# Kernel optimization log

Hardware: AMD Instinct MI355X
Metric: run time of the kernel (lower is better)

Reference implementation:

```python
import jax, jax.numpy as jnp
import numpy as np
from jax import lax

N, D, K = 8192, 512, 16
EPS = 1e-8


def _safe_sqrt(x):
    # sqrt with a guard so vjp is finite at exact zeros (diagonal of dist matrix)
    return jnp.where(x > 0, jnp.sqrt(jnp.maximum(x, 1e-12)), 0.0)


def _pairwise_dist(a):
    # [n, d] -> [n, n] euclidean distances via Gram trick
    sq = jnp.sum(a * a, axis=-1)
    d2 = sq[:, None] + sq[None, :] - 2.0 * (a @ a.T)
    return _safe_sqrt(d2)


def _curvature_proxy(emb, k):
    n = emb.shape[0]
    dists = _pairwise_dist(emb)  # [n, n]
    neg_d, knn_idx = lax.top_k(-dists, k + 1)  # k+1 smallest
    knn_dists = -neg_d[:, 1:]   # drop self [n, k]
    knn_idx = knn_idx[:, 1:]    # [n, k]
    avg_dist_to_neighbors = knn_dists.mean(axis=1)  # [n]

    nb = emb[knn_idx]  # [n, k, d] gathered neighbor embeddings
    nsq = jnp.sum(nb * nb, axis=-1)  # [n, k]
    gram = jnp.einsum('nkd,nld->nkl', nb, nb)  # [n, k, k]
    inter = _safe_sqrt(nsq[:, :, None] + nsq[:, None, :] - 2.0 * gram)

    mask = jnp.triu(jnp.ones((k, k), dtype=bool), 1)
    n_pairs = k * (k - 1) // 2
    inter_mean = jnp.sum(jnp.where(mask, inter, 0.0), axis=(1, 2)) / n_pairs  # [n]

    curvature = inter_mean / (avg_dist_to_neighbors + EPS)
    return curvature, knn_dists


def setup_inputs() -> dict:
    key = jax.random.key(0)
    k1, k2, k3 = jax.random.split(key, 3)
    embeddings = jax.random.normal(k1, (N, D), dtype=jnp.float32)
    ref_curvature = jax.random.uniform(k2, (N,), dtype=jnp.float32)
    ref_distances = jax.random.uniform(k3, (N, K), dtype=jnp.float32)
    return {"embeddings": embeddings, "ref_curvature": ref_curvature,
            "ref_distances": ref_distances}


def reference(embeddings, ref_curvature, ref_distances):
    curr_curv, curr_dists = _curvature_proxy(embeddings, K)
    curvature_loss = jnp.mean((curr_curv - ref_curvature) ** 2)
    scale_loss = (curr_dists.mean() - ref_distances.mean()) ** 2
    return curvature_loss + 0.1 * scale_loss
```

## Files before the change

### kernel.cpp

```cpp
#include <hip/hip_runtime.h>
#include <cfloat>
#include <cmath>
#include <stdint.h>

#define N 8192
#define D 512
#define K 16
#define RB 64
#define JS 2048
#define NSL (N / JS)
#define JT 128
#define NT (JS / JT)
#define KC 64
#define NCH (D / KC)
#define CAP 32
#define PB 64

typedef __bf16 bf16x8 __attribute__((ext_vector_type(8)));
typedef __bf16 bf16x4 __attribute__((ext_vector_type(4)));
typedef float  f32x16 __attribute__((ext_vector_type(16)));
typedef float  f32x4  __attribute__((ext_vector_type(4)));

__global__ __launch_bounds__(256)
void k_cast_sqnorm(const float* __restrict__ emb, float* __restrict__ sq,
                   __bf16* __restrict__ embh, int* __restrict__ kadjG) {
    int row = blockIdx.x * 4 + (threadIdx.x >> 6);
    int lane = threadIdx.x & 63;
    const float4* e = (const float4*)(emb + (size_t)row * D);
    float s = 0.f;
    #pragma unroll
    for (int c = 0; c < 2; c++) {
        float4 v = e[lane + 64 * c];
        s += v.x * v.x + v.y * v.y + v.z * v.z + v.w * v.w;
        bf16x4 h = { (__bf16)v.x, (__bf16)v.y, (__bf16)v.z, (__bf16)v.w };
        *(bf16x4*)&embh[(size_t)row * D + (size_t)(lane + 64 * c) * 4] = h;
    }
    for (int off = 32; off; off >>= 1) s += __shfl_down(s, off, 64);
    if (lane == 0) sq[row] = s;
    if (lane == 1) kadjG[row] = 0x7f7fffff;
}

__global__ __launch_bounds__(512)
void k_knn(const __bf16* __restrict__ embh, const float* __restrict__ sq,
           float* __restrict__ pd2, int* __restrict__ pidx,
           int* __restrict__ kadjG) {
    __shared__ __align__(16) __bf16 As[2][RB][KC + 8];
    __shared__ __align__(16) __bf16 Bs[2][JT][KC + 8];
    __shared__ float svD[RB][CAP + 1];
    __shared__ int   svI[RB][CAP + 1];
    __shared__ float sqr[RB];
    __shared__ float kadj[RB];
    __shared__ int   scount[RB];
    __shared__ int   again2[2];

    const int t   = threadIdx.x;
    const int rg  = blockIdx.x >> 2;
    const int sl  = blockIdx.x & 3;
    const int ib  = rg * RB;
    const int jsb = sl * JS;
    const int lane = t & 63, quad = lane >> 5, l31 = lane & 31;
    const int w  = t >> 6;
    const int wr = (w & 1) * 32;
    const int wc = (w >> 1) * 32;

    const int mrow = t >> 3, tid8 = t & 7;
    float l0 = FLT_MAX, l1 = FLT_MAX;
    int   i0 = 0, i1 = 0;
    float kmx = FLT_MAX;
    int   nfill = 0;

    if (t < RB) {
        sqr[t] = sq[ib + t];
        kadj[t] = FLT_MAX; scount[t] = 0;
    }
    __syncthreads();

    for (int jt = 0; jt < NT; jt++) {
        const int jb = jsb + jt * JT;
        f32x16 acc = {};

        {
            int row = t >> 3, g = t & 7;
            *(uint4*)&As[0][row][g * 8] = *(const uint4*)&embh[(size_t)(ib + row) * D + g * 8];
            #pragma unroll
            for (int q = 0; q < 2; q++) {
                int s = t + 512 * q;
                int brow = s >> 3, bg = s & 7;
                *(uint4*)&Bs[0][brow][bg * 8] = *(const uint4*)&embh[(size_t)(jb + brow) * D + bg * 8];
            }
        }
        __syncthreads();

        uint4 pfA, pfB[2];
        for (int kc = 0; kc < NCH; kc++) {
            const int cur = kc & 1;
            if (kc + 1 < NCH) {
                int k0 = (kc + 1) * KC;
                {
                    int row = t >> 3, g = t & 7;
                    pfA = *(const uint4*)&embh[(size_t)(ib + row) * D + k0 + g * 8];
                }
                #pragma unroll
                for (int q = 0; q < 2; q++) {
                    int s = t + 512 * q; int brow = s >> 3, bg = s & 7;
                    pfB[q] = *(const uint4*)&embh[(size_t)(jb + brow) * D + k0 + bg * 8];
                }
            }
            #pragma unroll
            for (int kk = 0; kk < KC / 16; kk++) {
                int ko = kk * 16 + quad * 8;
                bf16x8 a0 = *(const bf16x8*)&As[cur][wr + l31][ko];
                bf16x8 b0 = *(const bf16x8*)&Bs[cur][wc + l31][ko];
                acc = __builtin_amdgcn_mfma_f32_32x32x16_bf16(a0, b0, acc, 0, 0, 0);
            }
            if (kc + 1 < NCH) {
                {
                    int row = t >> 3, g = t & 7;
                    *(uint4*)&As[cur ^ 1][row][g * 8] = pfA;
                }
                #pragma unroll
                for (int q = 0; q < 2; q++) {
                    int s = t + 512 * q; int brow = s >> 3, bg = s & 7;
                    *(uint4*)&Bs[cur ^ 1][brow][bg * 8] = pfB[q];
                }
            }
            __syncthreads();
        }

        if (t < RB) {
            float g = __int_as_float(kadjG[ib + t]);
            kadj[t] = fminf(kadj[t], g - sqr[t]);
        }
        if (t == 0) again2[0] = 0;
        __syncthreads();

        float sqc0 = sq[jb + wc + l31];
        uint32_t mask = 0;
        int pass = 0;
        while (true) {
            #pragma unroll
            for (int reg = 0; reg < 16; reg++) {
                if ((mask >> reg) & 1) continue;
                int row_l = wr + ((reg & 3) + ((reg >> 2) << 3) + (quad << 2));
                float t2 = sqc0 - 2.f * acc[reg];
                if (t2 < kadj[row_l]) {
                    int j = jb + wc + l31;
                    if (j != ib + row_l) {
                        int p = atomicAdd(&scount[row_l], 1);
                        if (p < CAP) {
                            svD[row_l][p] = t2 + sqr[row_l];
                            svI[row_l][p] = j;
                            mask |= (1u << reg);
                        }
                    }
                }
            }
            __syncthreads();
            {
                int cnt = scount[mrow];
                if (cnt) {
                    int m = cnt < CAP ? cnt : CAP;
                    for (int p = 0; p < m; p++) {
                        float d2 = svD[mrow][p];
                        if (d2 < kmx) {
                            if (nfill < K) {
                                if ((nfill >> 1) == tid8) {
                                    int jv = svI[mrow][p];
                                    if ((nfill & 1) == 0) { l0 = d2; i0 = jv; }
                                    else                  { l1 = d2; i1 = jv; }
                                }
                                nfill++;
                                if (nfill == K) {
                                    float lm = fmaxf(l0, l1);
                                    #pragma unroll
                                    for (int off = 1; off < 8; off <<= 1)
                                        lm = fmaxf(lm, __shfl_xor(lm, off, 64));
                                    kmx = lm;
                                }
                            } else {
                                float mx = l0; int am = 0;
                                if (l1 > mx) { mx = l1; am = 1; }
                                int gam = (tid8 << 1) | am;
                                #pragma unroll
                                for (int off = 1; off < 8; off <<= 1) {
                                    float omx = __shfl_xor(mx, off, 64);
                                    int   oga = __shfl_xor(gam, off, 64);
                                    if (omx > mx || (omx == mx && oga < gam)) { mx = omx; gam = oga; }
                                }
                                if ((gam >> 1) == tid8) {
                                    int jv = svI[mrow][p];
                                    if ((gam & 1) == 0) { l0 = d2; i0 = jv; }
                                    else                { l1 = d2; i1 = jv; }
                                }
                                float lm = fmaxf(l0, l1);
                                #pragma unroll
                                for (int off = 1; off < 8; off <<= 1)
                                    lm = fmaxf(lm, __shfl_xor(lm, off, 64));
                                kmx = lm;
                            }
                        }
                    }
                    if (tid8 == 0) {
                        kadj[mrow] = fminf(kadj[mrow], kmx - sqr[mrow]);
                        scount[mrow] = 0;
                        if (cnt > CAP) again2[pass & 1] = 1;
                    }
                }
            }
            if (t == 0) again2[(pass + 1) & 1] = 0;
            __syncthreads();
            if (!again2[pass & 1]) break;
            pass++;
        }

        if (tid8 == 0 && kmx < FLT_MAX)
            atomicMin(&kadjG[ib + mrow], __float_as_int(kmx));
    }

    {
        size_t base = (size_t)(ib + mrow) * (NSL * K) + sl * K + tid8 * 2;
        pd2[base + 0] = l0; pd2[base + 1] = l1;
        pidx[base + 0] = i0; pidx[base + 1] = i1;
    }
}

__global__ __launch_bounds__(256)
void k_merge(const float* __restrict__ pd2, const int* __restrict__ pidx,
             int* __restrict__ knn, float* __restrict__ row_sum) {
    int row = blockIdx.x * 256 + threadIdx.x;
    float bd[K]; int bi[K];
    #pragma unroll
    for (int q = 0; q < K; q++) { bd[q] = FLT_MAX; bi[q] = 0; }
    float kmx = FLT_MAX;
    const float* pr = pd2 + (size_t)row * (NSL * K);
    const int*   pi = pidx + (size_t)row * (NSL * K);
    for (int s = 0; s < NSL * K; s++) {
        float d2 = pr[s];
        if (d2 < kmx) {
            int am = 0; float mx = bd[0];
            #pragma unroll
            for (int q = 1; q < K; q++) if (bd[q] > mx) { mx = bd[q]; am = q; }
            bd[am] = d2; bi[am] = pi[s];
            mx = bd[0];
            #pragma unroll
            for (int q = 1; q < K; q++) mx = fmaxf(mx, bd[q]);
            kmx = mx;
        }
    }
    float s = 0.f;
    #pragma unroll
    for (int q = 0; q < K; q++) {
        float d2 = bd[q];
        s += (d2 > 0.f) ? sqrtf(fmaxf(d2, 1e-12f)) : 0.f;
        knn[(size_t)row * K + q] = bi[q];
    }
    row_sum[row] = s;
}

__global__ __launch_bounds__(256)
void k_curv(const __bf16* __restrict__ embh, const int* __restrict__ knn_idx,
            const float* __restrict__ row_sum, const float* __restrict__ ref_curv,
            float* __restrict__ curv_err) {
    __shared__ float diagS[4][16];
    const int t = threadIdx.x;
    const int w = t >> 6, lane = t & 63;
    const int i = blockIdx.x * 4 + w;

    const int nidx = knn_idx[(size_t)i * K + (lane & 15)];
    const __bf16* src = embh + (size_t)nidx * D + (lane >> 4) * 8;

    f32x4 acc = {};
    #pragma unroll
    for (int kc = 0; kc < D / 32; kc++) {
        bf16x8 a = *(const bf16x8*)(src + kc * 32);
        acc = __builtin_amdgcn_mfma_f32_16x16x32_bf16(a, a, acc, 0, 0, 0);
    }

    #pragma unroll
    for (int q = 0; q < 4; q++) {
        int r = (lane >> 4) * 4 + q;
        if (r == (lane & 15)) diagS[w][r] = acc[q];
    }
    __syncthreads();

    float s = 0.f;
    #pragma unroll
    for (int q = 0; q < 4; q++) {
        int r = (lane >> 4) * 4 + q, c = lane & 15;
        if (r != c) {
            float d2 = diagS[w][r] + diagS[w][c] - 2.f * acc[q];
            s += (d2 > 0.f) ? sqrtf(fmaxf(d2, 1e-12f)) : 0.f;
        }
    }
    #pragma unroll
    for (int off = 32; off; off >>= 1) s += __shfl_down(s, off, 64);

    if (lane == 0) {
        float inter_mean = (0.5f * s) / 120.f;
        float avg = row_sum[i] / 16.f;
        float curv = inter_mean / (avg + 1e-8f);
        float diff = curv - ref_curv[i];
        curv_err[i] = diff * diff;
    }
}

__global__ __launch_bounds__(256)
void k_part(const float* __restrict__ curv_err, const float* __restrict__ row_sum,
            const float* __restrict__ ref_dist, float* __restrict__ part) {
    const int b = blockIdx.x, t = threadIdx.x;
    const int gid = b * 256 + t;
    const int stride = PB * 256;
    float s1 = 0.f, s2 = 0.f, s3 = 0.f;
    for (int i = gid; i < N; i += stride) { s1 += curv_err[i]; s2 += row_sum[i]; }
    for (int i = gid; i < N * K; i += stride) s3 += ref_dist[i];
    for (int off = 32; off; off >>= 1) {
        s1 += __shfl_down(s1, off, 64);
        s2 += __shfl_down(s2, off, 64);
        s3 += __shfl_down(s3, off, 64);
    }
    __shared__ float a1[4], a2[4], a3[4];
    int w = t >> 6, lane = t & 63;
    if (lane == 0) { a1[w] = s1; a2[w] = s2; a3[w] = s3; }
    __syncthreads();
    if (t == 0) {
        float t1 = 0.f, t2 = 0.f, t3 = 0.f;
        #pragma unroll
        for (int q = 0; q < 4; q++) { t1 += a1[q]; t2 += a2[q]; t3 += a3[q]; }
        part[b] = t1; part[PB + b] = t2; part[2 * PB + b] = t3;
    }
}

__global__ __launch_bounds__(64)
void k_final2(const float* __restrict__ part, float* __restrict__ out) {
    const int t = threadIdx.x;
    float s1 = part[t], s2 = part[PB + t], s3 = part[2 * PB + t];
    for (int off = 32; off; off >>= 1) {
        s1 += __shfl_down(s1, off, 64);
        s2 += __shfl_down(s2, off, 64);
        s3 += __shfl_down(s3, off, 64);
    }
    if (t == 0) {
        float curv_loss = s1 / (float)N;
        float dm = s2 / (float)(N * K);
        float rm = s3 / (float)(N * K);
        float d = dm - rm;
        out[0] = curv_loss + 0.1f * d * d;
    }
}

extern "C" void kernel_launch(void* const* d_in, const int* in_sizes, int n_in,
                              void* d_out, int out_size, void* d_ws, size_t ws_size,
                              hipStream_t stream) {
    const float* emb      = (const float*)d_in[0];
    const float* ref_curv = (const float*)d_in[1];
    const float* ref_dist = (const float*)d_in[2];
    float* out = (float*)d_out;

    float*  sq       = (float*)d_ws;
    float*  row_sum  = sq + N;
    float*  curv_err = row_sum + N;
    float*  pd2      = curv_err + N;
    int*    pidx     = (int*)(pd2 + (size_t)N * NSL * K);
    int*    knn      = pidx + (size_t)N * NSL * K;
    __bf16* embh     = (__bf16*)(knn + (size_t)N * K);
    float*  part     = (float*)(embh + (size_t)N * D);
    int*    kadjG    = (int*)(part + 3 * PB);

    k_cast_sqnorm<<<N / 4, 256, 0, stream>>>(emb, sq, embh, kadjG);
    k_knn<<<(N / RB) * NSL, 512, 0, stream>>>(embh, sq, pd2, pidx, kadjG);
    k_merge<<<N / 256, 256, 0, stream>>>(pd2, pidx, knn, row_sum);
    k_curv<<<N / 4, 256, 0, stream>>>(embh, knn, row_sum, ref_curv, curv_err);
    k_part<<<PB, 256, 0, stream>>>(curv_err, row_sum, ref_dist, part);
    k_final2<<<1, 64, 0, stream>>>(part, out);
}
```

Measured before the change: 369.3 us.

## Widen KNN column tile to 256 and prefetch across tiles with single-buffered B

Doubles the column tile so each wave computes two 32x32 MFMA accumulators that share one A fragment, which doubles reuse of A reads from shared memory. B is now single-buffered with an extra barrier, and the global prefetch runs across tile boundaries so the next tile's first chunk is loaded during the current tile's last chunk. This removes the per-tile reload stall. In exchange it adds a second barrier per k-chunk, more registers for the doubled accumulators and prefetch buffers, and a 64-bit candidate mask.

Result: slower. 726.0 us (+96.6%).

```diff
diff --git a/kernel.cpp b/kernel.cpp
--- a/kernel.cpp
+++ b/kernel.cpp
@@ -9,7 +9,7 @@
 #define RB 64
 #define JS 2048
 #define NSL (N / JS)
-#define JT 128
+#define JT 256
 #define NT (JS / JT)
 #define KC 64
 #define NCH (D / KC)
@@ -45,7 +45,7 @@
            float* __restrict__ pd2, int* __restrict__ pidx,
            int* __restrict__ kadjG) {
     __shared__ __align__(16) __bf16 As[2][RB][KC + 8];
-    __shared__ __align__(16) __bf16 Bs[2][JT][KC + 8];
+    __shared__ __align__(16) __bf16 Bs[JT][KC + 8];
     __shared__ float svD[RB][CAP + 1];
     __shared__ int   svI[RB][CAP + 1];
     __shared__ float sqr[RB];
@@ -61,7 +61,9 @@
     const int lane = t & 63, quad = lane >> 5, l31 = lane & 31;
     const int w  = t >> 6;
     const int wr = (w & 1) * 32;
-    const int wc = (w >> 1) * 32;
+    const int wc = (w >> 1) * 64;
+
+    const int arow = t >> 3, ag = t & 7;
 
     const int mrow = t >> 3, tid8 = t & 7;
     float l0 = FLT_MAX, l1 = FLT_MAX;
@@ -73,58 +75,57 @@
         sqr[t] = sq[ib + t];
         kadj[t] = FLT_MAX; scount[t] = 0;
     }
+
+    {
+        *(uint4*)&As[0][arow][ag * 8] = *(const uint4*)&embh[(size_t)(ib + arow) * D + ag * 8];
+        #pragma unroll
+        for (int q = 0; q < 4; q++) {
+            int s = t + 512 * q;
+            int brow = s >> 3, bg = s & 7;
+            *(uint4*)&Bs[brow][bg * 8] = *(const uint4*)&embh[(size_t)(jsb + brow) * D + bg * 8];
+        }
+    }
     __syncthreads();
 
+    int cb = 0;
     for (int jt = 0; jt < NT; jt++) {
         const int jb = jsb + jt * JT;
-        f32x16 acc = {};
-
-        {
-            int row = t >> 3, g = t & 7;
-            *(uint4*)&As[0][row][g * 8] = *(const uint4*)&embh[(size_t)(ib + row) * D + g * 8];
-            #pragma unroll
-            for (int q = 0; q < 2; q++) {
-                int s = t + 512 * q;
-                int brow = s >> 3, bg = s & 7;
-                *(uint4*)&Bs[0][brow][bg * 8] = *(const uint4*)&embh[(size_t)(jb + brow) * D + bg * 8];
-            }
-        }
-        __syncthreads();
-
-        uint4 pfA, pfB[2];
+        f32x16 acc[2];
+        acc[0] = (f32x16){}; acc[1] = (f32x16){};
+
         for (int kc = 0; kc < NCH; kc++) {
-            const int cur = kc & 1;
-            if (kc + 1 < NCH) {
-                int k0 = (kc + 1) * KC;
-                {
-                    int row = t >> 3, g = t & 7;
-                    pfA = *(const uint4*)&embh[(size_t)(ib + row) * D + k0 + g * 8];
-                }
+            const bool has_next = (kc + 1 < NCH) || (jt + 1 < NT);
+            uint4 pfA, pfB[4];
+            if (has_next) {
+                const int nk0 = (kc + 1 < NCH) ? (kc + 1) * KC : 0;
+                const int njb = (kc + 1 < NCH) ? jb : jb + JT;
+                pfA = *(const uint4*)&embh[(size_t)(ib + arow) * D + nk0 + ag * 8];
                 #pragma unroll
-                for (int q = 0; q < 2; q++) {
+                for (int q = 0; q < 4; q++) {
                     int s = t + 512 * q; int brow = s >> 3, bg = s & 7;
-                    pfB[q] = *(const uint4*)&embh[(size_t)(jb + brow) * D + k0 + bg * 8];
+                    pfB[q] = *(const uint4*)&embh[(size_t)(njb + brow) * D + nk0 + bg * 8];
                 }
             }
             #pragma unroll
             for (int kk = 0; kk < KC / 16; kk++) {
                 int ko = kk * 16 + quad * 8;
-                bf16x8 a0 = *(const bf16x8*)&As[cur][wr + l31][ko];
-                bf16x8 b0 = *(const bf16x8*)&Bs[cur][wc + l31][ko];
-                acc = __builtin_amdgcn_mfma_f32_32x32x16_bf16(a0, b0, acc, 0, 0, 0);
-            }
-            if (kc + 1 < NCH) {
-                {
-                    int row = t >> 3, g = t & 7;
-                    *(uint4*)&As[cur ^ 1][row][g * 8] = pfA;
+                bf16x8 a0 = *(const bf16x8*)&As[cb][wr + l31][ko];
+                bf16x8 b0 = *(const bf16x8*)&Bs[wc + l31][ko];
+                bf16x8 b1 = *(const bf16x8*)&Bs[wc + 32 + l31][ko];
+                acc[0] = __builtin_amdgcn_mfma_f32_32x32x16_bf16(a0, b0, acc[0], 0, 0, 0);
+                acc[1] = __builtin_amdgcn_mfma_f32_32x32x16_bf16(a0, b1, acc[1], 0, 0, 0);
+            }
+            __syncthreads();
+            if (has_next) {
+                *(uint4*)&As[cb ^ 1][arow][ag * 8] = pfA;
+                #pragma unroll
+                for (int q = 0; q < 4; q++) {
+                    int s = t + 512 * q; int brow = s >> 3, bg = s & 7;
+                    *(uint4*)&Bs[brow][bg * 8] = pfB[q];
                 }
-                #pragma unroll
-                for (int q = 0; q < 2; q++) {
-                    int s = t + 512 * q; int brow = s >> 3, bg = s & 7;
-                    *(uint4*)&Bs[cur ^ 1][brow][bg * 8] = pfB[q];
-                }
             }
             __syncthreads();
+            cb ^= 1;
         }
 
         if (t < RB) {
@@ -135,22 +136,26 @@
         __syncthreads();
 
         float sqc0 = sq[jb + wc + l31];
-        uint32_t mask = 0;
+        float sqc1 = sq[jb + wc + 32 + l31];
+        uint64_t mask = 0;
         int pass = 0;
         while (true) {
             #pragma unroll
+            for (int c = 0; c < 2; c++)
+            #pragma unroll
             for (int reg = 0; reg < 16; reg++) {
-                if ((mask >> reg) & 1) continue;
+                int bit = (c << 4) | reg;
+                if ((mask >> bit) & 1) continue;
                 int row_l = wr + ((reg & 3) + ((reg >> 2) << 3) + (quad << 2));
-                float t2 = sqc0 - 2.f * acc[reg];
+                float t2 = (c ? sqc1 : sqc0) - 2.f * acc[c][reg];
                 if (t2 < kadj[row_l]) {
-                    int j = jb + wc + l31;
+                    int j = jb + wc + c * 32 + l31;
                     if (j != ib + row_l) {
                         int p = atomicAdd(&scount[row_l], 1);
                         if (p < CAP) {
                             svD[row_l][p] = t2 + sqr[row_l];
                             svI[row_l][p] = j;
-                            mask |= (1u << reg);
+                            mask |= (1ull << bit);
                         }
                     }
                 }
```

## Batch two column tiles per selection pass and fuse merge into curvature kernel

Applied to the files above, without the earlier changes.

The kNN kernel now computes two 128-column GEMM tiles into separate accumulators before each candidate-selection pass. This halves the number of selection passes and their barriers, at the cost of doubled accumulator registers and a 32-bit mask. MFMA sections are wrapped in s_setprio to favor the matrix work. The separate top-k merge kernel is folded into the curvature kernel: every lane redundantly merges the 64 candidates for its row, which removes a launch and the knn index round-trip but makes each wave do the merge 64 times over.

After: 580.8 us. 57.3% more time.

```diff
diff --git a/kernel.cpp b/kernel.cpp
--- a/kernel.cpp
+++ b/kernel.cpp
@@ -75,56 +75,63 @@
     }
     __syncthreads();
 
-    for (int jt = 0; jt < NT; jt++) {
-        const int jb = jsb + jt * JT;
-        f32x16 acc = {};
-
-        {
-            int row = t >> 3, g = t & 7;
-            *(uint4*)&As[0][row][g * 8] = *(const uint4*)&embh[(size_t)(ib + row) * D + g * 8];
-            #pragma unroll
-            for (int q = 0; q < 2; q++) {
-                int s = t + 512 * q;
-                int brow = s >> 3, bg = s & 7;
-                *(uint4*)&Bs[0][brow][bg * 8] = *(const uint4*)&embh[(size_t)(jb + brow) * D + bg * 8];
-            }
-        }
-        __syncthreads();
-
-        uint4 pfA, pfB[2];
-        for (int kc = 0; kc < NCH; kc++) {
-            const int cur = kc & 1;
-            if (kc + 1 < NCH) {
-                int k0 = (kc + 1) * KC;
-                {
-                    int row = t >> 3, g = t & 7;
-                    pfA = *(const uint4*)&embh[(size_t)(ib + row) * D + k0 + g * 8];
-                }
+    for (int jp = 0; jp < NT; jp += 2) {
+        f32x16 acc[2];
+
+        #pragma unroll
+        for (int half = 0; half < 2; half++) {
+            const int jb = jsb + (jp + half) * JT;
+            acc[half] = (f32x16){};
+
+            {
+                int row = t >> 3, g = t & 7;
+                *(uint4*)&As[0][row][g * 8] = *(const uint4*)&embh[(size_t)(ib + row) * D + g * 8];
                 #pragma unroll
                 for (int q = 0; q < 2; q++) {
-                    int s = t + 512 * q; int brow = s >> 3, bg = s & 7;
-                    pfB[q] = *(const uint4*)&embh[(size_t)(jb + brow) * D + k0 + bg * 8];
-                }
-            }
-            #pragma unroll
-            for (int kk = 0; kk < KC / 16; kk++) {
-                int ko = kk * 16 + quad * 8;
-                bf16x8 a0 = *(const bf16x8*)&As[cur][wr + l31][ko];
-                bf16x8 b0 = *(const bf16x8*)&Bs[cur][wc + l31][ko];
-                acc = __builtin_amdgcn_mfma_f32_32x32x16_bf16(a0, b0, acc, 0, 0, 0);
-            }
-            if (kc + 1 < NCH) {
-                {
-                    int row = t >> 3, g = t & 7;
-                    *(uint4*)&As[cur ^ 1][row][g * 8] = pfA;
-                }
-                #pragma unroll
-                for (int q = 0; q < 2; q++) {
-                    int s = t + 512 * q; int brow = s >> 3, bg = s & 7;
-                    *(uint4*)&Bs[cur ^ 1][brow][bg * 8] = pfB[q];
+                    int s = t + 512 * q;
+                    int brow = s >> 3, bg = s & 7;
+                    *(uint4*)&Bs[0][brow][bg * 8] = *(const uint4*)&embh[(size_t)(jb + brow) * D + bg * 8];
                 }
             }
             __syncthreads();
+
+            uint4 pfA, pfB[2];
+            for (int kc = 0; kc < NCH; kc++) {
+                const int cur = kc & 1;
+                if (kc + 1 < NCH) {
+                    int k0 = (kc + 1) * KC;
+                    {
+                        int row = t >> 3, g = t & 7;
+                        pfA = *(const uint4*)&embh[(size_t)(ib + row) * D + k0 + g * 8];
+                    }
+                    #pragma unroll
+                    for (int q = 0; q < 2; q++) {
+                        int s = t + 512 * q; int brow = s >> 3, bg = s & 7;
+                        pfB[q] = *(const uint4*)&embh[(size_t)(jb + brow) * D + k0 + bg * 8];
+                    }
+                }
+                __builtin_amdgcn_s_setprio(1);
+                #pragma unroll
+                for (int kk = 0; kk < KC / 16; kk++) {
+                    int ko = kk * 16 + quad * 8;
+                    bf16x8 a0 = *(const bf16x8*)&As[cur][wr + l31][ko];
+                    bf16x8 b0 = *(const bf16x8*)&Bs[cur][wc + l31][ko];
+                    acc[half] = __builtin_amdgcn_mfma_f32_32x32x16_bf16(a0, b0, acc[half], 0, 0, 0);
+                }
+                __builtin_amdgcn_s_setprio(0);
+                if (kc + 1 < NCH) {
+                    {
+                        int row = t >> 3, g = t & 7;
+                        *(uint4*)&As[cur ^ 1][row][g * 8] = pfA;
+                    }
+                    #pragma unroll
+                    for (int q = 0; q < 2; q++) {
+                        int s = t + 512 * q; int brow = s >> 3, bg = s & 7;
+                        *(uint4*)&Bs[cur ^ 1][brow][bg * 8] = pfB[q];
+                    }
+                }
+                __syncthreads();
+            }
         }
 
         if (t < RB) {
@@ -134,23 +141,28 @@
         if (t == 0) again2[0] = 0;
         __syncthreads();
 
-        float sqc0 = sq[jb + wc + l31];
+        const int jb0 = jsb + jp * JT, jb1 = jb0 + JT;
+        float sqc0 = sq[jb0 + wc + l31];
+        float sqc1 = sq[jb1 + wc + l31];
         uint32_t mask = 0;
         int pass = 0;
         while (true) {
             #pragma unroll
+            for (int h = 0; h < 2; h++)
+            #pragma unroll
             for (int reg = 0; reg < 16; reg++) {
-                if ((mask >> reg) & 1) continue;
+                int bit = (h << 4) | reg;
+                if ((mask >> bit) & 1) continue;
                 int row_l = wr + ((reg & 3) + ((reg >> 2) << 3) + (quad << 2));
-                float t2 = sqc0 - 2.f * acc[reg];
+                float t2 = (h ? sqc1 : sqc0) - 2.f * acc[h][reg];
                 if (t2 < kadj[row_l]) {
-                    int j = jb + wc + l31;
+                    int j = (h ? jb1 : jb0) + wc + l31;
                     if (j != ib + row_l) {
                         int p = atomicAdd(&scount[row_l], 1);
                         if (p < CAP) {
                             svD[row_l][p] = t2 + sqr[row_l];
                             svI[row_l][p] = j;
-                            mask |= (1u << reg);
+                            mask |= (1u << bit);
                         }
                     }
                 }
@@ -225,15 +237,20 @@
 }
 
 __global__ __launch_bounds__(256)
-void k_merge(const float* __restrict__ pd2, const int* __restrict__ pidx,
-             int* __restrict__ knn, float* __restrict__ row_sum) {
-    int row = blockIdx.x * 256 + threadIdx.x;
+void k_curvm(const __bf16* __restrict__ embh, const float* __restrict__ pd2,
+             const int* __restrict__ pidx, const float* __restrict__ ref_curv,
+             float* __restrict__ curv_err, float* __restrict__ row_sum) {
+    __shared__ float diagS[4][16];
+    const int t = threadIdx.x;
+    const int w = t >> 6, lane = t & 63;
+    const int i = blockIdx.x * 4 + w;
+
     float bd[K]; int bi[K];
     #pragma unroll
     for (int q = 0; q < K; q++) { bd[q] = FLT_MAX; bi[q] = 0; }
     float kmx = FLT_MAX;
-    const float* pr = pd2 + (size_t)row * (NSL * K);
-    const int*   pi = pidx + (size_t)row * (NSL * K);
+    const float* pr = pd2 + (size_t)i * (NSL * K);
+    const int*   pi = pidx + (size_t)i * (NSL * K);
     for (int s = 0; s < NSL * K; s++) {
         float d2 = pr[s];
         if (d2 < kmx) {
@@ -247,28 +264,19 @@
             kmx = mx;
         }
     }
-    float s = 0.f;
+    float rs = 0.f;
     #pragma unroll
     for (int q = 0; q < K; q++) {
         float d2 = bd[q];
-        s += (d2 > 0.f) ? sqrtf(fmaxf(d2, 1e-12f)) : 0.f;
-        knn[(size_t)row * K + q] = bi[q];
-    }
-    row_sum[row] = s;
-}
-
-__global__ __launch_bounds__(256)
-void k_curv(const __bf16* __restrict__ embh, const int* __restrict__ knn_idx,
-            const float* __restrict__ row_sum, const float* __restrict__ ref_curv,
-            float* __restrict__ curv_err) {
-    __shared__ float diagS[4][16];
-    const int t = threadIdx.x;
-    const int w = t >> 6, lane = t & 63;
-    const int i = blockIdx.x * 4 + w;
-
-    const int nidx = knn_idx[(size_t)i * K + (lane & 15)];
+        rs += (d2 > 0.f) ? sqrtf(fmaxf(d2, 1e-12f)) : 0.f;
+    }
+    if (lane == 0) row_sum[i] = rs;
+
+    int nidx = bi[0];
+    #pragma unroll
+    for (int q = 1; q < K; q++) if ((lane & 15) == q) nidx = bi[q];
+
     const __bf16* src = embh + (size_t)nidx * D + (lane >> 4) * 8;
-
     f32x4 acc = {};
     #pragma unroll
     for (int kc = 0; kc < D / 32; kc++) {
@@ -297,7 +305,7 @@
 
     if (lane == 0) {
         float inter_mean = (0.5f * s) / 120.f;
-        float avg = row_sum[i] / 16.f;
+        float avg = rs / 16.f;
         float curv = inter_mean / (avg + 1e-8f);
         float diff = curv - ref_curv[i];
         curv_err[i] = diff * diff;
@@ -361,15 +369,13 @@
     float*  curv_err = row_sum + N;
     float*  pd2      = curv_err + N;
     int*    pidx     = (int*)(pd2 + (size_t)N * NSL * K);
-    int*    knn      = pidx + (size_t)N * NSL * K;
-    __bf16* embh     = (__bf16*)(knn + (size_t)N * K);
+    __bf16* embh     = (__bf16*)(pidx + (size_t)N * NSL * K);
     float*  part     = (float*)(embh + (size_t)N * D);
     int*    kadjG    = (int*)(part + 3 * PB);
 
     k_cast_sqnorm<<<N / 4, 256, 0, stream>>>(emb, sq, embh, kadjG);
     k_knn<<<(N / RB) * NSL, 512, 0, stream>>>(embh, sq, pd2, pidx, kadjG);
-    k_merge<<<N / 256, 256, 0, stream>>>(pd2, pidx, knn, row_sum);
-    k_curv<<<N / 4, 256, 0, stream>>>(embh, knn, row_sum, ref_curv, curv_err);
+    k_curvm<<<N / 4, 256, 0, stream>>>(embh, pd2, pidx, ref_curv, curv_err, row_sum);
     k_part<<<PB, 256, 0, stream>>>(curv_err, row_sum, ref_dist, part);
     k_final2<<<1, 64, 0, stream>>>(part, out);
 }
```
